# Performance work log

Hardware: AMD Instinct MI355X
Metric: run time of the kernel (lower is better)

Reference implementation:

```python
import jax, jax.numpy as jnp
import numpy as np

N_NODES = 100000
N_EDGES = 3200000
F_IN = 128
CHANNELS = 128


def setup_inputs() -> dict:
    key = jax.random.key(0)
    k1, k2, k3, k4, k5 = jax.random.split(key, 5)
    x = jax.random.normal(k1, (N_NODES, F_IN), dtype=jnp.float32)
    kernel = jax.random.normal(k2, (F_IN, CHANNELS), dtype=jnp.float32) * (1.0 / np.sqrt(F_IN))
    bias = jnp.zeros((CHANNELS,), dtype=jnp.float32)
    edge_row = jnp.sort(jax.random.randint(k3, (N_EDGES,), 0, N_NODES, dtype=jnp.int32))
    edge_col = jax.random.randint(k4, (N_EDGES,), 0, N_NODES, dtype=jnp.int32)
    edge_val = jax.random.uniform(k5, (N_EDGES,), dtype=jnp.float32)
    return {"x": x, "kernel": kernel, "bias": bias, "edge_val": edge_val,
            "edge_row": edge_row, "edge_col": edge_col}


def reference(x, kernel, bias, edge_val, edge_row, edge_col):
    # Z = relu(A_tilde @ (X @ W) + b), A_tilde given in COO form (row, col, val)
    n = x.shape[0]
    xw = x @ kernel                              # [N, C] dense projection
    msgs = xw[edge_col] * edge_val[:, None]      # [E, C] gather + scale
    agg = jax.ops.segment_sum(msgs, edge_row, num_segments=n)  # SpMM scatter
    return jax.nn.relu(agg + bias)
```

## Files before the change

### kernel.cpp

```cpp
#include <hip/hip_runtime.h>

#define F_IN 128
#define CH   128

typedef __attribute__((ext_vector_type(8))) short bf16x8;
typedef __attribute__((ext_vector_type(4))) float f32x4;
typedef __attribute__((ext_vector_type(2))) float f32x2;
typedef __attribute__((ext_vector_type(2))) unsigned u32x2;

static __device__ __forceinline__ ushort f2b(float f) {
  union { float f; unsigned u; } v; v.f = f;
  const unsigned u = v.u;
  return (ushort)((u + 0x7FFFu + ((u >> 16) & 1u)) >> 16);
}

__global__ __launch_bounds__(512) void gemm_rowptr_fused(
    const float* __restrict__ x, const float* __restrict__ w,
    unsigned char* __restrict__ xwq, float* __restrict__ scale,
    const int* __restrict__ edge_row, int* __restrict__ row_ptr,
    int n, int n_edges, int gemm_blocks) {
  __shared__ __align__(16) ushort Wt[F_IN * CH];
  const int t = threadIdx.x;

  if ((int)blockIdx.x >= gemm_blocks) {
    const int r = ((int)blockIdx.x - gemm_blocks) * 512 + t;
    if (r <= n) {
      int lo = 0, hi = n_edges;
      while (lo < hi) {
        const int mid = (lo + hi) >> 1;
        if (edge_row[mid] < r) lo = mid + 1; else hi = mid;
      }
      row_ptr[r] = lo;
    }
    return;
  }

  for (int i = t; i < (F_IN * CH) / 4; i += 512) {
    const int k  = i >> 5;
    const int n4 = (i & 31) << 2;
    const f32x4 wv = *(const f32x4*)&w[k * CH + n4];
#pragma unroll
    for (int q = 0; q < 4; ++q) {
      const int nn = n4 + q;
      const int byte = (nn * 256 + k * 2) ^ ((nn & 7) << 4);
      *(ushort*)((char*)Wt + byte) = f2b(wv[q]);
    }
  }
  __syncthreads();

  const int wave = t >> 6, lane = t & 63;
  const int R0   = blockIdx.x * 128 + wave * 16;
  const int arow = R0 + (lane & 15);
  const int kgrp = (lane >> 4) * 8;

  bf16x8 a[4];
#pragma unroll
  for (int s = 0; s < 4; ++s) {
    if (arow < n) {
      const f32x4 p0 = __builtin_nontemporal_load(
          (const f32x4*)&x[arow * F_IN + s * 32 + kgrp]);
      const f32x4 p1 = __builtin_nontemporal_load(
          (const f32x4*)&x[arow * F_IN + s * 32 + kgrp + 4]);
#pragma unroll
      for (int j = 0; j < 4; ++j) {
        a[s][j]     = (short)f2b(p0[j]);
        a[s][j + 4] = (short)f2b(p1[j]);
      }
    } else {
#pragma unroll
      for (int j = 0; j < 8; ++j) a[s][j] = (short)0;
    }
  }

  f32x4 acc[8];
#pragma unroll
  for (int t8 = 0; t8 < 8; ++t8) acc[t8] = (f32x4){0.f, 0.f, 0.f, 0.f};

#pragma unroll
  for (int t8 = 0; t8 < 8; ++t8) {
    const int col = t8 * 16 + (lane & 15);
#pragma unroll
    for (int s = 0; s < 4; ++s) {
      const int byte = (col * 256 + (s * 32 + kgrp) * 2) ^ ((col & 7) << 4);
      const bf16x8 b = *(const bf16x8*)((const char*)Wt + byte);
      acc[t8] = __builtin_amdgcn_mfma_f32_16x16x32_bf16(a[s], b, acc[t8], 0, 0, 0);
    }
  }

  const int li = lane & 15;
  const int r0 = R0 + (lane >> 4) * 4;
#pragma unroll
  for (int i = 0; i < 4; ++i) {
    const int rr = r0 + i;
    float m = 0.f;
#pragma unroll
    for (int t8 = 0; t8 < 8; ++t8) m = fmaxf(m, fabsf(acc[t8][i]));
    m = fmaxf(m, __shfl_xor(m, 1));
    m = fmaxf(m, __shfl_xor(m, 2));
    m = fmaxf(m, __shfl_xor(m, 4));
    m = fmaxf(m, __shfl_xor(m, 8));
    const float inv = (m > 1e-20f) ? 127.f / m : 0.f;
    if (rr < n) {
      if (li == 0) scale[rr] = m * (1.f / 127.f);
#pragma unroll
      for (int t8 = 0; t8 < 8; ++t8) {
        const float q = rintf(acc[t8][i] * inv) + 128.f;
        xwq[rr * CH + t8 * 16 + li] = (unsigned char)q;
      }
    }
  }
}

#define ACCD(word, j0, vv)                                                \
  do {                                                                    \
    f32x2 lo_, hi_;                                                       \
    lo_[0] = (float)((word) & 0xFFu);                                     \
    lo_[1] = (float)(((word) >> 8) & 0xFFu);                              \
    hi_[0] = (float)(((word) >> 16) & 0xFFu);                             \
    hi_[1] = (float)((word) >> 24);                                       \
    acc2[(j0)]     = __builtin_elementwise_fma(vv, lo_, acc2[(j0)]);      \
    acc2[(j0) + 1] = __builtin_elementwise_fma(vv, hi_, acc2[(j0) + 1]);  \
  } while (0)

#define ACC8PK(U, V)                                                      \
  do {                                                                    \
    const f32x2 vv_ = {(V), (V)};                                         \
    ACCD((U)[0], 0, vv_);                                                 \
    ACCD((U)[1], 2, vv_);                                                 \
  } while (0)

__global__ __launch_bounds__(256) void spmm_qwave(
    const unsigned char* __restrict__ xwq, const float* __restrict__ scale,
    const float* __restrict__ edge_val, const int* __restrict__ edge_col,
    const int* __restrict__ row_ptr, const float* __restrict__ bias,
    float* __restrict__ out, int n) {
  __shared__ int   cbuf[256];
  __shared__ float vbuf[256];
  const int tid = threadIdx.x;
  const int row = (int)((blockIdx.x * 256 + tid) >> 4);
  if (row >= n) return;
  const int li    = tid & 15;
  const int qbase = tid & ~15;
  const u32x2* __restrict__ xw2 = (const u32x2*)xwq;

  const int start = row_ptr[row], end = row_ptr[row + 1];

  f32x2 acc2[4];
#pragma unroll
  for (int j = 0; j < 4; ++j) acc2[j] = (f32x2){0.f, 0.f};
  float S = 0.f;

  for (int e0 = start; e0 < end; e0 += 16) {
    const int e = e0 + li;
    int   c_my = 0;
    float vp_my = 0.f;
    if (e < end) {
      c_my = __builtin_nontemporal_load(edge_col + e);
      vp_my = __builtin_nontemporal_load(edge_val + e) * scale[c_my];
    }
    S += vp_my;
    cbuf[tid] = c_my;
    vbuf[tid] = vp_my;

    u32x2 u[16];
#pragma unroll
    for (int it4 = 0; it4 < 4; ++it4) {
      const int4 c4 = *(const int4*)&cbuf[qbase + it4 * 4];
      u[it4 * 4 + 0] = xw2[c4.x * 16 + li];
      u[it4 * 4 + 1] = xw2[c4.y * 16 + li];
      u[it4 * 4 + 2] = xw2[c4.z * 16 + li];
      u[it4 * 4 + 3] = xw2[c4.w * 16 + li];
    }

#pragma unroll
    for (int it4 = 0; it4 < 4; ++it4) {
      const f32x4 v4 = *(const f32x4*)&vbuf[qbase + it4 * 4];
      ACC8PK(u[it4 * 4 + 0], v4[0]);
      ACC8PK(u[it4 * 4 + 1], v4[1]);
      ACC8PK(u[it4 * 4 + 2], v4[2]);
      ACC8PK(u[it4 * 4 + 3], v4[3]);
    }
  }

  S += __shfl_xor(S, 1);
  S += __shfl_xor(S, 2);
  S += __shfl_xor(S, 4);
  S += __shfl_xor(S, 8);

  const float off = 128.f * S;
  const float* a = (const float*)acc2;
  const int cb = li * 8;
  const f32x4 b0 = *(const f32x4*)&bias[cb];
  const f32x4 b1 = *(const f32x4*)&bias[cb + 4];
  f32x4 o0, o1;
  o0[0] = fmaxf(a[0] - off + b0[0], 0.f);
  o0[1] = fmaxf(a[1] - off + b0[1], 0.f);
  o0[2] = fmaxf(a[2] - off + b0[2], 0.f);
  o0[3] = fmaxf(a[3] - off + b0[3], 0.f);
  o1[0] = fmaxf(a[4] - off + b1[0], 0.f);
  o1[1] = fmaxf(a[5] - off + b1[1], 0.f);
  o1[2] = fmaxf(a[6] - off + b1[2], 0.f);
  o1[3] = fmaxf(a[7] - off + b1[3], 0.f);
  __builtin_nontemporal_store(o0, (f32x4*)&out[(size_t)row * CH + cb]);
  __builtin_nontemporal_store(o1, (f32x4*)&out[(size_t)row * CH + cb + 4]);
}

extern "C" void kernel_launch(void* const* d_in, const int* in_sizes, int n_in,
                              void* d_out, int out_size, void* d_ws, size_t ws_size,
                              hipStream_t stream) {
  const float* x        = (const float*)d_in[0];
  const float* kernel   = (const float*)d_in[1];
  const float* bias     = (const float*)d_in[2];
  const float* edge_val = (const float*)d_in[3];
  const int*   edge_row = (const int*)d_in[4];
  const int*   edge_col = (const int*)d_in[5];
  float* out = (float*)d_out;

  const int n       = in_sizes[0] / F_IN;
  const int n_edges = in_sizes[3];

  unsigned char* xwq = (unsigned char*)d_ws;
  float* scale = (float*)((char*)d_ws + (size_t)n * CH);
  int* rowptr  = (int*)((char*)d_ws + (size_t)n * CH + (size_t)n * sizeof(float));

  const int GB = (n + 127) / 128;
  const int RB = (n + 1 + 511) / 512;
  gemm_rowptr_fused<<<GB + RB, 512, 0, stream>>>(x, kernel, xwq, scale,
                                                 edge_row, rowptr,
                                                 n, n_edges, GB);

  const int blocks = (n * 16 + 255) / 256;
  spmm_qwave<<<blocks, 256, 0, stream>>>(xwq, scale, edge_val, edge_col,
                                         rowptr, bias, out, n);
}
```

Baseline: 112.5 us.

## Prefetch next edge chunk in SpMM and process two row groups per GEMM block

The SpMM loop now loads the next 16 edges' column indices, values and scale products while the current chunk's gathers and FMAs run, software-pipelining the dependent index-then-gather chain. The GEMM blocks each handle 256 rows in two passes, so the bf16 conversion of W into shared memory is amortized over twice as many rows and half as many blocks are launched. The costs are higher register pressure in SpMM, fewer GEMM blocks to spread across CUs, and serialized work inside each GEMM block.

```diff
diff --git a/kernel.cpp b/kernel.cpp
--- a/kernel.cpp
+++ b/kernel.cpp
@@ -49,63 +49,66 @@
   __syncthreads();
 
   const int wave = t >> 6, lane = t & 63;
-  const int R0   = blockIdx.x * 128 + wave * 16;
-  const int arow = R0 + (lane & 15);
+  const int li   = lane & 15;
   const int kgrp = (lane >> 4) * 8;
 
-  bf16x8 a[4];
-#pragma unroll
-  for (int s = 0; s < 4; ++s) {
-    if (arow < n) {
-      const f32x4 p0 = __builtin_nontemporal_load(
-          (const f32x4*)&x[arow * F_IN + s * 32 + kgrp]);
-      const f32x4 p1 = __builtin_nontemporal_load(
-          (const f32x4*)&x[arow * F_IN + s * 32 + kgrp + 4]);
-#pragma unroll
-      for (int j = 0; j < 4; ++j) {
-        a[s][j]     = (short)f2b(p0[j]);
-        a[s][j + 4] = (short)f2b(p1[j]);
-      }
-    } else {
-#pragma unroll
-      for (int j = 0; j < 8; ++j) a[s][j] = (short)0;
-    }
-  }
-
-  f32x4 acc[8];
-#pragma unroll
-  for (int t8 = 0; t8 < 8; ++t8) acc[t8] = (f32x4){0.f, 0.f, 0.f, 0.f};
-
-#pragma unroll
-  for (int t8 = 0; t8 < 8; ++t8) {
-    const int col = t8 * 16 + (lane & 15);
+  for (int grp = 0; grp < 2; ++grp) {
+    const int R0   = blockIdx.x * 256 + grp * 128 + wave * 16;
+    const int arow = R0 + li;
+
+    bf16x8 a[4];
 #pragma unroll
     for (int s = 0; s < 4; ++s) {
-      const int byte = (col * 256 + (s * 32 + kgrp) * 2) ^ ((col & 7) << 4);
-      const bf16x8 b = *(const bf16x8*)((const char*)Wt + byte);
-      acc[t8] = __builtin_amdgcn_mfma_f32_16x16x32_bf16(a[s], b, acc[t8], 0, 0, 0);
-    }
-  }
-
-  const int li = lane & 15;
-  const int r0 = R0 + (lane >> 4) * 4;
-#pragma unroll
-  for (int i = 0; i < 4; ++i) {
-    const int rr = r0 + i;
-    float m = 0.f;
-#pragma unroll
-    for (int t8 = 0; t8 < 8; ++t8) m = fmaxf(m, fabsf(acc[t8][i]));
-    m = fmaxf(m, __shfl_xor(m, 1));
-    m = fmaxf(m, __shfl_xor(m, 2));
-    m = fmaxf(m, __shfl_xor(m, 4));
-    m = fmaxf(m, __shfl_xor(m, 8));
-    const float inv = (m > 1e-20f) ? 127.f / m : 0.f;
-    if (rr < n) {
-      if (li == 0) scale[rr] = m * (1.f / 127.f);
-#pragma unroll
-      for (int t8 = 0; t8 < 8; ++t8) {
-        const float q = rintf(acc[t8][i] * inv) + 128.f;
-        xwq[rr * CH + t8 * 16 + li] = (unsigned char)q;
+      if (arow < n) {
+        const f32x4 p0 = __builtin_nontemporal_load(
+            (const f32x4*)&x[arow * F_IN + s * 32 + kgrp]);
+        const f32x4 p1 = __builtin_nontemporal_load(
+            (const f32x4*)&x[arow * F_IN + s * 32 + kgrp + 4]);
+#pragma unroll
+        for (int j = 0; j < 4; ++j) {
+          a[s][j]     = (short)f2b(p0[j]);
+          a[s][j + 4] = (short)f2b(p1[j]);
+        }
+      } else {
+#pragma unroll
+        for (int j = 0; j < 8; ++j) a[s][j] = (short)0;
+      }
+    }
+
+    f32x4 acc[8];
+#pragma unroll
+    for (int t8 = 0; t8 < 8; ++t8) acc[t8] = (f32x4){0.f, 0.f, 0.f, 0.f};
+
+#pragma unroll
+    for (int t8 = 0; t8 < 8; ++t8) {
+      const int col = t8 * 16 + li;
+#pragma unroll
+      for (int s = 0; s < 4; ++s) {
+        const int byte = (col * 256 + (s * 32 + kgrp) * 2) ^ ((col & 7) << 4);
+        const bf16x8 b = *(const bf16x8*)((const char*)Wt + byte);
+        acc[t8] = __builtin_amdgcn_mfma_f32_16x16x32_bf16(a[s], b, acc[t8], 0, 0, 0);
+      }
+    }
+
+    const int r0 = R0 + (lane >> 4) * 4;
+#pragma unroll
+    for (int i = 0; i < 4; ++i) {
+      const int rr = r0 + i;
+      float m = 0.f;
+#pragma unroll
+      for (int t8 = 0; t8 < 8; ++t8) m = fmaxf(m, fabsf(acc[t8][i]));
+      m = fmaxf(m, __shfl_xor(m, 1));
+      m = fmaxf(m, __shfl_xor(m, 2));
+      m = fmaxf(m, __shfl_xor(m, 4));
+      m = fmaxf(m, __shfl_xor(m, 8));
+      const float inv = (m > 1e-20f) ? 127.f / m : 0.f;
+      if (rr < n) {
+        if (li == 0) scale[rr] = m * (1.f / 127.f);
+#pragma unroll
+        for (int t8 = 0; t8 < 8; ++t8) {
+          const float q = rintf(acc[t8][i] * inv) + 128.f;
+          xwq[rr * CH + t8 * 16 + li] = (unsigned char)q;
+        }
       }
     }
   }
@@ -150,17 +153,20 @@
   for (int j = 0; j < 4; ++j) acc2[j] = (f32x2){0.f, 0.f};
   float S = 0.f;
 
+  int   c_cur = 0;
+  float vp_cur = 0.f;
+  {
+    const int e = start + li;
+    if (e < end) {
+      c_cur = __builtin_nontemporal_load(edge_col + e);
+      vp_cur = __builtin_nontemporal_load(edge_val + e) * scale[c_cur];
+    }
+  }
+
   for (int e0 = start; e0 < end; e0 += 16) {
-    const int e = e0 + li;
-    int   c_my = 0;
-    float vp_my = 0.f;
-    if (e < end) {
-      c_my = __builtin_nontemporal_load(edge_col + e);
-      vp_my = __builtin_nontemporal_load(edge_val + e) * scale[c_my];
-    }
-    S += vp_my;
-    cbuf[tid] = c_my;
-    vbuf[tid] = vp_my;
+    S += vp_cur;
+    cbuf[tid] = c_cur;
+    vbuf[tid] = vp_cur;
 
     u32x2 u[16];
 #pragma unroll
@@ -172,6 +178,16 @@
       u[it4 * 4 + 3] = xw2[c4.w * 16 + li];
     }
 
+    int   c_nxt = 0;
+    float vp_nxt = 0.f;
+    {
+      const int en = e0 + 16 + li;
+      if (en < end) {
+        c_nxt = __builtin_nontemporal_load(edge_col + en);
+        vp_nxt = __builtin_nontemporal_load(edge_val + en) * scale[c_nxt];
+      }
+    }
+
 #pragma unroll
     for (int it4 = 0; it4 < 4; ++it4) {
       const f32x4 v4 = *(const f32x4*)&vbuf[qbase + it4 * 4];
@@ -180,6 +196,9 @@
       ACC8PK(u[it4 * 4 + 2], v4[2]);
       ACC8PK(u[it4 * 4 + 3], v4[3]);
     }
+
+    c_cur = c_nxt;
+    vp_cur = vp_nxt;
   }
 
   S += __shfl_xor(S, 1);
@@ -223,7 +242,7 @@
   float* scale = (float*)((char*)d_ws + (size_t)n * CH);
   int* rowptr  = (int*)((char*)d_ws + (size_t)n * CH + (size_t)n * sizeof(float));
 
-  const int GB = (n + 127) / 128;
+  const int GB = (n + 255) / 256;
   const int RB = (n + 1 + 511) / 512;
   gemm_rowptr_fused<<<GB + RB, 512, 0, stream>>>(x, kernel, xwq, scale,
                                                  edge_row, rowptr,
```

After: 114.1 us. Within noise of the previous version (+1.4%).

## Use 8 lanes per row with 16-byte gathers and edge-parallel row_ptr build

Applied to the files above, without the earlier changes.

The SpMM kernel now gives each row 8 lanes instead of 16, and each lane gathers 16 quantized bytes per edge as a single 128-bit load, processing 8 edges per iteration. This halves the thread count and doubles the bytes per load, trading some latency hiding for fewer wider memory transactions. The row_ptr construction changes from a per-row binary search over edge_row to an edge-parallel boundary scan, where each edge writes the row_ptr entries between its row and the next edge's row. That scan reads edge_row once, coalesced, but launches many more blocks (one thread per edge).

```diff
diff --git a/kernel.cpp b/kernel.cpp
--- a/kernel.cpp
+++ b/kernel.cpp
@@ -6,7 +6,7 @@
 typedef __attribute__((ext_vector_type(8))) short bf16x8;
 typedef __attribute__((ext_vector_type(4))) float f32x4;
 typedef __attribute__((ext_vector_type(2))) float f32x2;
-typedef __attribute__((ext_vector_type(2))) unsigned u32x2;
+typedef __attribute__((ext_vector_type(4))) unsigned u32x4;
 
 static __device__ __forceinline__ ushort f2b(float f) {
   union { float f; unsigned u; } v; v.f = f;
@@ -23,14 +23,14 @@
   const int t = threadIdx.x;
 
   if ((int)blockIdx.x >= gemm_blocks) {
-    const int r = ((int)blockIdx.x - gemm_blocks) * 512 + t;
-    if (r <= n) {
-      int lo = 0, hi = n_edges;
-      while (lo < hi) {
-        const int mid = (lo + hi) >> 1;
-        if (edge_row[mid] < r) lo = mid + 1; else hi = mid;
+    const int e = ((int)blockIdx.x - gemm_blocks) * 512 + t;
+    if (e < n_edges) {
+      const int a = edge_row[e];
+      const int b = (e + 1 < n_edges) ? edge_row[e + 1] : n;
+      if (e == 0) {
+        for (int r = 0; r <= a; ++r) row_ptr[r] = 0;
       }
-      row_ptr[r] = lo;
+      for (int r = a + 1; r <= b; ++r) row_ptr[r] = e + 1;
     }
     return;
   }
@@ -49,9 +49,10 @@
   __syncthreads();
 
   const int wave = t >> 6, lane = t & 63;
+  const int li   = lane & 15;
+  const int kgrp = (lane >> 4) * 8;
   const int R0   = blockIdx.x * 128 + wave * 16;
-  const int arow = R0 + (lane & 15);
-  const int kgrp = (lane >> 4) * 8;
+  const int arow = R0 + li;
 
   bf16x8 a[4];
 #pragma unroll
@@ -78,7 +79,7 @@
 
 #pragma unroll
   for (int t8 = 0; t8 < 8; ++t8) {
-    const int col = t8 * 16 + (lane & 15);
+    const int col = t8 * 16 + li;
 #pragma unroll
     for (int s = 0; s < 4; ++s) {
       const int byte = (col * 256 + (s * 32 + kgrp) * 2) ^ ((col & 7) << 4);
@@ -87,7 +88,6 @@
     }
   }
 
-  const int li = lane & 15;
   const int r0 = R0 + (lane >> 4) * 4;
 #pragma unroll
   for (int i = 0; i < 4; ++i) {
@@ -122,14 +122,16 @@
     acc2[(j0) + 1] = __builtin_elementwise_fma(vv, hi_, acc2[(j0) + 1]);  \
   } while (0)
 
-#define ACC8PK(U, V)                                                      \
+#define ACC16PK(U, V)                                                     \
   do {                                                                    \
     const f32x2 vv_ = {(V), (V)};                                         \
     ACCD((U)[0], 0, vv_);                                                 \
     ACCD((U)[1], 2, vv_);                                                 \
+    ACCD((U)[2], 4, vv_);                                                 \
+    ACCD((U)[3], 6, vv_);                                                 \
   } while (0)
 
-__global__ __launch_bounds__(256) void spmm_qwave(
+__global__ __launch_bounds__(256) void spmm_owave(
     const unsigned char* __restrict__ xwq, const float* __restrict__ scale,
     const float* __restrict__ edge_val, const int* __restrict__ edge_col,
     const int* __restrict__ row_ptr, const float* __restrict__ bias,
@@ -137,21 +139,21 @@
   __shared__ int   cbuf[256];
   __shared__ float vbuf[256];
   const int tid = threadIdx.x;
-  const int row = (int)((blockIdx.x * 256 + tid) >> 4);
+  const int row = (int)((blockIdx.x * 256 + tid) >> 3);
   if (row >= n) return;
-  const int li    = tid & 15;
-  const int qbase = tid & ~15;
-  const u32x2* __restrict__ xw2 = (const u32x2*)xwq;
+  const int l8    = tid & 7;
+  const int obase = tid & ~7;
+  const u32x4* __restrict__ xw4 = (const u32x4*)xwq;
 
   const int start = row_ptr[row], end = row_ptr[row + 1];
 
-  f32x2 acc2[4];
-#pragma unroll
-  for (int j = 0; j < 4; ++j) acc2[j] = (f32x2){0.f, 0.f};
+  f32x2 acc2[8];
+#pragma unroll
+  for (int j = 0; j < 8; ++j) acc2[j] = (f32x2){0.f, 0.f};
   float S = 0.f;
 
-  for (int e0 = start; e0 < end; e0 += 16) {
-    const int e = e0 + li;
+  for (int e0 = start; e0 < end; e0 += 8) {
+    const int e = e0 + l8;
     int   c_my = 0;
     float vp_my = 0.f;
     if (e < end) {
@@ -162,47 +164,47 @@
     cbuf[tid] = c_my;
     vbuf[tid] = vp_my;
 
-    u32x2 u[16];
-#pragma unroll
-    for (int it4 = 0; it4 < 4; ++it4) {
-      const int4 c4 = *(const int4*)&cbuf[qbase + it4 * 4];
-      u[it4 * 4 + 0] = xw2[c4.x * 16 + li];
-      u[it4 * 4 + 1] = xw2[c4.y * 16 + li];
-      u[it4 * 4 + 2] = xw2[c4.z * 16 + li];
-      u[it4 * 4 + 3] = xw2[c4.w * 16 + li];
-    }
-
-#pragma unroll
-    for (int it4 = 0; it4 < 4; ++it4) {
-      const f32x4 v4 = *(const f32x4*)&vbuf[qbase + it4 * 4];
-      ACC8PK(u[it4 * 4 + 0], v4[0]);
-      ACC8PK(u[it4 * 4 + 1], v4[1]);
-      ACC8PK(u[it4 * 4 + 2], v4[2]);
-      ACC8PK(u[it4 * 4 + 3], v4[3]);
-    }
+    const int4 ca = *(const int4*)&cbuf[obase];
+    const int4 cb = *(const int4*)&cbuf[obase + 4];
+    u32x4 u[8];
+    u[0] = xw4[ca.x * 8 + l8];
+    u[1] = xw4[ca.y * 8 + l8];
+    u[2] = xw4[ca.z * 8 + l8];
+    u[3] = xw4[ca.w * 8 + l8];
+    u[4] = xw4[cb.x * 8 + l8];
+    u[5] = xw4[cb.y * 8 + l8];
+    u[6] = xw4[cb.z * 8 + l8];
+    u[7] = xw4[cb.w * 8 + l8];
+
+    const f32x4 va = *(const f32x4*)&vbuf[obase];
+    const f32x4 vb = *(const f32x4*)&vbuf[obase + 4];
+    ACC16PK(u[0], va[0]);
+    ACC16PK(u[1], va[1]);
+    ACC16PK(u[2], va[2]);
+    ACC16PK(u[3], va[3]);
+    ACC16PK(u[4], vb[0]);
+    ACC16PK(u[5], vb[1]);
+    ACC16PK(u[6], vb[2]);
+    ACC16PK(u[7], vb[3]);
   }
 
   S += __shfl_xor(S, 1);
   S += __shfl_xor(S, 2);
   S += __shfl_xor(S, 4);
-  S += __shfl_xor(S, 8);
 
   const float off = 128.f * S;
   const float* a = (const float*)acc2;
-  const int cb = li * 8;
-  const f32x4 b0 = *(const f32x4*)&bias[cb];
-  const f32x4 b1 = *(const f32x4*)&bias[cb + 4];
-  f32x4 o0, o1;
-  o0[0] = fmaxf(a[0] - off + b0[0], 0.f);
-  o0[1] = fmaxf(a[1] - off + b0[1], 0.f);
-  o0[2] = fmaxf(a[2] - off + b0[2], 0.f);
-  o0[3] = fmaxf(a[3] - off + b0[3], 0.f);
-  o1[0] = fmaxf(a[4] - off + b1[0], 0.f);
-  o1[1] = fmaxf(a[5] - off + b1[1], 0.f);
-  o1[2] = fmaxf(a[6] - off + b1[2], 0.f);
-  o1[3] = fmaxf(a[7] - off + b1[3], 0.f);
-  __builtin_nontemporal_store(o0, (f32x4*)&out[(size_t)row * CH + cb]);
-  __builtin_nontemporal_store(o1, (f32x4*)&out[(size_t)row * CH + cb + 4]);
+  const int cb0 = l8 * 16;
+#pragma unroll
+  for (int q = 0; q < 4; ++q) {
+    const f32x4 bv = *(const f32x4*)&bias[cb0 + q * 4];
+    f32x4 o;
+    o[0] = fmaxf(a[q * 4 + 0] - off + bv[0], 0.f);
+    o[1] = fmaxf(a[q * 4 + 1] - off + bv[1], 0.f);
+    o[2] = fmaxf(a[q * 4 + 2] - off + bv[2], 0.f);
+    o[3] = fmaxf(a[q * 4 + 3] - off + bv[3], 0.f);
+    __builtin_nontemporal_store(o, (f32x4*)&out[(size_t)row * CH + cb0 + q * 4]);
+  }
 }
 
 extern "C" void kernel_launch(void* const* d_in, const int* in_sizes, int n_in,
@@ -224,12 +226,12 @@
   int* rowptr  = (int*)((char*)d_ws + (size_t)n * CH + (size_t)n * sizeof(float));
 
   const int GB = (n + 127) / 128;
-  const int RB = (n + 1 + 511) / 512;
+  const int RB = (n_edges + 511) / 512;
   gemm_rowptr_fused<<<GB + RB, 512, 0, stream>>>(x, kernel, xwq, scale,
                                                  edge_row, rowptr,
                                                  n, n_edges, GB);
 
-  const int blocks = (n * 16 + 255) / 256;
-  spmm_qwave<<<blocks, 256, 0, stream>>>(xwq, scale, edge_val, edge_col,
+  const int blocks = (n * 8 + 255) / 256;
+  spmm_owave<<<blocks, 256, 0, stream>>>(xwq, scale, edge_val, edge_col,
                                          rowptr, bias, out, n);
 }
```

New measurement: 125.3 us. 11.3% more time.

## Build row_ptr via per-edge boundary scan and widen SpMM edge batch to 32

Applied to the files above, without the earlier changes.

Row-pointer construction switches from a per-row binary search over edge_row to a per-edge pass in which each edge writes the row_ptr entries between its row and the next edge's row. This removes the log-depth dependent loads of the search but launches one thread per edge instead of one per row. The SpMM loop now stages 32 edges per iteration instead of 16, issuing twice as many independent gathers before accumulating and skipping empty 8-edge groups. The wider batch raises register pressure and wastes more lanes on rows with short edge lists.

```diff
diff --git a/kernel.cpp b/kernel.cpp
--- a/kernel.cpp
+++ b/kernel.cpp
@@ -23,14 +23,14 @@
   const int t = threadIdx.x;
 
   if ((int)blockIdx.x >= gemm_blocks) {
-    const int r = ((int)blockIdx.x - gemm_blocks) * 512 + t;
-    if (r <= n) {
-      int lo = 0, hi = n_edges;
-      while (lo < hi) {
-        const int mid = (lo + hi) >> 1;
-        if (edge_row[mid] < r) lo = mid + 1; else hi = mid;
+    const int e = ((int)blockIdx.x - gemm_blocks) * 512 + t;
+    if (e < n_edges) {
+      const int a = edge_row[e];
+      const int b = (e + 1 < n_edges) ? edge_row[e + 1] : n;
+      if (e == 0) {
+        for (int r = 0; r <= a; ++r) row_ptr[r] = 0;
       }
-      row_ptr[r] = lo;
+      for (int r = a + 1; r <= b; ++r) row_ptr[r] = e + 1;
     }
     return;
   }
@@ -49,9 +49,10 @@
   __syncthreads();
 
   const int wave = t >> 6, lane = t & 63;
+  const int li   = lane & 15;
+  const int kgrp = (lane >> 4) * 8;
   const int R0   = blockIdx.x * 128 + wave * 16;
-  const int arow = R0 + (lane & 15);
-  const int kgrp = (lane >> 4) * 8;
+  const int arow = R0 + li;
 
   bf16x8 a[4];
 #pragma unroll
@@ -78,7 +79,7 @@
 
 #pragma unroll
   for (int t8 = 0; t8 < 8; ++t8) {
-    const int col = t8 * 16 + (lane & 15);
+    const int col = t8 * 16 + li;
 #pragma unroll
     for (int s = 0; s < 4; ++s) {
       const int byte = (col * 256 + (s * 32 + kgrp) * 2) ^ ((col & 7) << 4);
@@ -87,7 +88,6 @@
     }
   }
 
-  const int li = lane & 15;
   const int r0 = R0 + (lane >> 4) * 4;
 #pragma unroll
   for (int i = 0; i < 4; ++i) {
@@ -134,13 +134,13 @@
     const float* __restrict__ edge_val, const int* __restrict__ edge_col,
     const int* __restrict__ row_ptr, const float* __restrict__ bias,
     float* __restrict__ out, int n) {
-  __shared__ int   cbuf[256];
-  __shared__ float vbuf[256];
+  __shared__ int   cbuf[512];
+  __shared__ float vbuf[512];
   const int tid = threadIdx.x;
   const int row = (int)((blockIdx.x * 256 + tid) >> 4);
   if (row >= n) return;
-  const int li    = tid & 15;
-  const int qbase = tid & ~15;
+  const int li = tid & 15;
+  const int qb = (tid & ~15) * 2;
   const u32x2* __restrict__ xw2 = (const u32x2*)xwq;
 
   const int start = row_ptr[row], end = row_ptr[row + 1];
@@ -150,22 +150,26 @@
   for (int j = 0; j < 4; ++j) acc2[j] = (f32x2){0.f, 0.f};
   float S = 0.f;
 
-  for (int e0 = start; e0 < end; e0 += 16) {
-    const int e = e0 + li;
-    int   c_my = 0;
-    float vp_my = 0.f;
-    if (e < end) {
-      c_my = __builtin_nontemporal_load(edge_col + e);
-      vp_my = __builtin_nontemporal_load(edge_val + e) * scale[c_my];
-    }
-    S += vp_my;
-    cbuf[tid] = c_my;
-    vbuf[tid] = vp_my;
-
-    u32x2 u[16];
-#pragma unroll
-    for (int it4 = 0; it4 < 4; ++it4) {
-      const int4 c4 = *(const int4*)&cbuf[qbase + it4 * 4];
+  for (int e0 = start; e0 < end; e0 += 32) {
+    const int ea = e0 + li, eb = e0 + 16 + li;
+    int   c0 = 0, c1 = 0;
+    float v0 = 0.f, v1 = 0.f;
+    if (ea < end) {
+      c0 = __builtin_nontemporal_load(edge_col + ea);
+      v0 = __builtin_nontemporal_load(edge_val + ea) * scale[c0];
+    }
+    if (eb < end) {
+      c1 = __builtin_nontemporal_load(edge_col + eb);
+      v1 = __builtin_nontemporal_load(edge_val + eb) * scale[c1];
+    }
+    S += v0 + v1;
+    cbuf[qb + li] = c0;  cbuf[qb + 16 + li] = c1;
+    vbuf[qb + li] = v0;  vbuf[qb + 16 + li] = v1;
+
+    u32x2 u[32];
+#pragma unroll
+    for (int it4 = 0; it4 < 8; ++it4) {
+      const int4 c4 = *(const int4*)&cbuf[qb + it4 * 4];
       u[it4 * 4 + 0] = xw2[c4.x * 16 + li];
       u[it4 * 4 + 1] = xw2[c4.y * 16 + li];
       u[it4 * 4 + 2] = xw2[c4.z * 16 + li];
@@ -173,12 +177,18 @@
     }
 
 #pragma unroll
-    for (int it4 = 0; it4 < 4; ++it4) {
-      const f32x4 v4 = *(const f32x4*)&vbuf[qbase + it4 * 4];
-      ACC8PK(u[it4 * 4 + 0], v4[0]);
-      ACC8PK(u[it4 * 4 + 1], v4[1]);
-      ACC8PK(u[it4 * 4 + 2], v4[2]);
-      ACC8PK(u[it4 * 4 + 3], v4[3]);
+    for (int g = 0; g < 4; ++g) {
+      if (e0 + g * 8 >= end) break;
+      const f32x4 va = *(const f32x4*)&vbuf[qb + g * 8];
+      const f32x4 vb = *(const f32x4*)&vbuf[qb + g * 8 + 4];
+      ACC8PK(u[g * 8 + 0], va[0]);
+      ACC8PK(u[g * 8 + 1], va[1]);
+      ACC8PK(u[g * 8 + 2], va[2]);
+      ACC8PK(u[g * 8 + 3], va[3]);
+      ACC8PK(u[g * 8 + 4], vb[0]);
+      ACC8PK(u[g * 8 + 5], vb[1]);
+      ACC8PK(u[g * 8 + 6], vb[2]);
+      ACC8PK(u[g * 8 + 7], vb[3]);
     }
   }
 
@@ -224,7 +234,7 @@
   int* rowptr  = (int*)((char*)d_ws + (size_t)n * CH + (size_t)n * sizeof(float));
 
   const int GB = (n + 127) / 128;
-  const int RB = (n + 1 + 511) / 512;
+  const int RB = (n_edges + 511) / 512;
   gemm_rowptr_fused<<<GB + RB, 512, 0, stream>>>(x, kernel, xwq, scale,
                                                  edge_row, rowptr,
                                                  n, n_edges, GB);
```

After: 110.4 us. Within noise of the previous version (-1.9%).
